# Optimization experiments

Hardware: AMD Instinct MI355X
Metric: run time of the kernel (lower is better)

The kernel has to match this reference:

```python
import jax, jax.numpy as jnp
import numpy as np

B, N, L, D, KQ, OUT = 256, 256, 1024, 256, 64, 64


def setup_inputs() -> dict:
    key = jax.random.key(0)
    ks = jax.random.split(key, 6)
    return {
        "queries": jax.random.normal(ks[0], (B, D), dtype=jnp.float32),
        "keys": jax.random.normal(ks[1], (N, L, D), dtype=jnp.float32),
        "values": jax.random.normal(ks[2], (N, L, D), dtype=jnp.float32),
        "Wq": jax.random.normal(ks[3], (D, KQ), dtype=jnp.float32) * (1.0 / np.sqrt(D)),
        "Wk": jax.random.normal(ks[4], (D, KQ), dtype=jnp.float32) * (1.0 / np.sqrt(D)),
        "Wv": jax.random.normal(ks[5], (D, OUT), dtype=jnp.float32) * (1.0 / np.sqrt(D)),
    }


def reference(queries, keys, values, Wq, Wk, Wv):
    # Projections (bias-free Linear layers)
    q = queries @ Wq                          # [B, KQ]
    k = jnp.einsum('nld,dk->nlk', keys, Wk)   # [N, L, KQ]
    v = jnp.einsum('nld,do->nlo', values, Wv) # [N, L, OUT]
    scale = jnp.asarray(1.0 / np.sqrt(k.shape[-1]), dtype=q.dtype)
    # attn[n, b, l] = q[b] . k[n, l]
    attn = jnp.einsum('bk,nlk->nbl', q, k) * scale
    attn = jax.nn.softmax(attn, axis=-1)      # softmax over protein length L
    # Vectorized version of the per-drug bmm loop: result[b, n, :] = attn[n, b, :] @ v[n]
    result = jnp.einsum('nbl,nlo->bno', attn, v)  # [B, N, OUT]
    return (result, attn)
```

## Files before the change

### kernel.cpp

```cpp
#include <hip/hip_runtime.h>
#include <stdint.h>
#include <stddef.h>

#define B_ 256
#define N_ 256
#define L_ 1024
#define D_ 256
#define KQ_ 64
#define OUT_ 64
#define RESULT_ELEMS (256 * 256 * 64)

typedef __attribute__((ext_vector_type(4))) float f32x4;
typedef __attribute__((ext_vector_type(8))) short s16x8;
typedef __attribute__((ext_vector_type(4))) short s16x4;

__device__ __forceinline__ short f2bf(float f) {
  union { float f; unsigned int u; } v;
  v.f = f;
  unsigned int u = v.u;
  unsigned int r = (u + 0x7FFFu + ((u >> 16) & 1u)) >> 16;
  return (short)r;
}

__global__ void qproj_kernel(const float* __restrict__ queries,
                             const float* __restrict__ Wq,
                             float* __restrict__ qtmp) {
  int b = blockIdx.x * 4 + (threadIdx.x >> 6);
  int j = threadIdx.x & 63;
  float s = 0.f;
#pragma unroll 4
  for (int d = 0; d < D_; ++d)
    s += queries[b * D_ + d] * Wq[d * KQ_ + j];
  qtmp[b * KQ_ + j] = s * 0.125f;
}

__global__ void packq_kernel(const float* __restrict__ qtmp,
                             short* __restrict__ qfrag) {
  int bt = blockIdx.x >> 1, ks = blockIdx.x & 1;
  int lane = threadIdx.x, quad = lane >> 4, l15 = lane & 15;
  s16x8 v;
#pragma unroll
  for (int jj = 0; jj < 8; ++jj)
    v[jj] = f2bf(qtmp[(bt * 16 + l15) * KQ_ + ks * 32 + quad * 8 + jj]);
  *(s16x8*)(qfrag + ((size_t)(bt * 2 + ks) * 64 + lane) * 8) = v;
}

__global__ void packw_kernel(const float* __restrict__ Wk,
                             const float* __restrict__ Wv,
                             short* __restrict__ wkf, short* __restrict__ wvf) {
  int task = blockIdx.x >> 5;
  int ks = (blockIdx.x >> 2) & 7, ct = blockIdx.x & 3;
  const float* W = task ? Wv : Wk;
  short* dst = task ? wvf : wkf;
  int lane = threadIdx.x, quad = lane >> 4, l15 = lane & 15;
  s16x8 v;
#pragma unroll
  for (int jj = 0; jj < 8; ++jj)
    v[jj] = f2bf(W[(ks * 32 + quad * 8 + jj) * 64 + ct * 16 + l15]);
  *(s16x8*)(dst + ((size_t)(ks * 4 + ct) * 64 + lane) * 8) = v;
}

__global__ __launch_bounds__(256) void kvproj_kernel(
    const float* __restrict__ keys, const float* __restrict__ values,
    const short* __restrict__ wkf, const short* __restrict__ wvf,
    short* __restrict__ kfrag, short* __restrict__ vfrag) {
  __shared__ short lbuf[64 * 72];
  int task = blockIdx.y;
  const float* X = task ? values : keys;
  const short* wf = task ? wvf : wkf;
  int m0 = blockIdx.x * 64;
  int w = threadIdx.x >> 6, lane = threadIdx.x & 63;
  int quad = lane >> 4, l15 = lane & 15;

  f32x4 zero = {0.f, 0.f, 0.f, 0.f};
  f32x4 acc[4] = {zero, zero, zero, zero};

  const float* aptr = X + (size_t)(m0 + w * 16 + l15) * D_ + quad * 8;
#pragma unroll
  for (int ks = 0; ks < 8; ++ks) {
    f32x4 a0 = *(const f32x4*)(aptr + ks * 32);
    f32x4 a1 = *(const f32x4*)(aptr + ks * 32 + 4);
    s16x8 af;
#pragma unroll
    for (int jj = 0; jj < 4; ++jj) {
      af[jj] = f2bf(a0[jj]);
      af[jj + 4] = f2bf(a1[jj]);
    }
#pragma unroll
    for (int ct = 0; ct < 4; ++ct) {
      s16x8 bf = *(const s16x8*)(wf + ((size_t)(ks * 4 + ct) * 64 + lane) * 8);
      acc[ct] = __builtin_amdgcn_mfma_f32_16x16x32_bf16(af, bf, acc[ct], 0, 0, 0);
    }
  }

  int n = m0 >> 10, l0 = m0 & 1023;
  if (task == 0) {
#pragma unroll
    for (int ct = 0; ct < 4; ++ct)
#pragma unroll
      for (int r = 0; r < 4; ++r)
        lbuf[(w * 16 + quad * 4 + r) * 72 + ct * 16 + l15] = f2bf(acc[ct][r]);
    __syncthreads();
#pragma unroll
    for (int i = 0; i < 2; ++i) {
      int lt = w, ks = i;
      s16x8 v = *(const s16x8*)&lbuf[(lt * 16 + l15) * 72 + ks * 32 + quad * 8];
      size_t off = (((size_t)(n * 64 + (l0 >> 4) + lt) * 2 + ks) * 64 + lane) * 8;
      *(s16x8*)(kfrag + off) = v;
    }
  } else {
#pragma unroll
    for (int ct = 0; ct < 4; ++ct) {
      s16x4 p;
#pragma unroll
      for (int r = 0; r < 4; ++r) p[r] = f2bf(acc[ct][r]);
      *(s16x4*)&lbuf[(ct * 16 + l15) * 72 + w * 16 + quad * 4] = p;
    }
    __syncthreads();
#pragma unroll
    for (int i = 0; i < 2; ++i) {
      int fid = w * 2 + i, ls = fid >> 2, ot = fid & 3;
      s16x8 v = *(const s16x8*)&lbuf[(ot * 16 + l15) * 72 + ls * 32 + quad * 8];
      size_t off = (((size_t)(n * 32 + (l0 >> 5) + ls) * 4 + ot) * 64 + lane) * 8;
      *(s16x8*)(vfrag + off) = v;
    }
  }
}

__global__ __launch_bounds__(512) void attn_kernel(
    const short* __restrict__ qfrag, const short* __restrict__ kfrag,
    const short* __restrict__ vfrag, float* __restrict__ out) {
  __shared__ short tbuf[8 * 1280];
  int n = blockIdx.x;
  int w = threadIdx.x >> 6, lane = threadIdx.x & 63;
  int quad = lane >> 4, l15 = lane & 15;
  short* tb = tbuf + w * 1280;

  f32x4 zero = {0.f, 0.f, 0.f, 0.f};

  s16x8 qf[2][2];
#pragma unroll
  for (int bt = 0; bt < 2; ++bt)
#pragma unroll
    for (int ks = 0; ks < 2; ++ks)
      qf[bt][ks] = *(const s16x8*)(qfrag +
          ((size_t)((w * 2 + bt) * 2 + ks) * 64 + lane) * 8);

  const short* kb = kfrag + (size_t)n * 65536;
  const short* vb = vfrag + (size_t)n * 65536;

  float se[2][4] = {{0.f, 0.f, 0.f, 0.f}, {0.f, 0.f, 0.f, 0.f}};
#pragma unroll 2
  for (int c = 0; c < 32; ++c) {
    f32x4 S[2][2] = {{zero, zero}, {zero, zero}};
#pragma unroll
    for (int lt = 0; lt < 2; ++lt)
#pragma unroll
      for (int ks = 0; ks < 2; ++ks) {
        s16x8 kf = *(const s16x8*)(kb +
            ((size_t)((c * 2 + lt) * 2 + ks) * 64 + lane) * 8);
#pragma unroll
        for (int bt = 0; bt < 2; ++bt)
          S[bt][lt] = __builtin_amdgcn_mfma_f32_16x16x32_bf16(
              qf[bt][ks], kf, S[bt][lt], 0, 0, 0);
      }
#pragma unroll
    for (int bt = 0; bt < 2; ++bt)
#pragma unroll
      for (int lt = 0; lt < 2; ++lt)
#pragma unroll
        for (int r = 0; r < 4; ++r)
          se[bt][r] += __expf(S[bt][lt][r]);
  }
#pragma unroll
  for (int bt = 0; bt < 2; ++bt)
#pragma unroll
    for (int r = 0; r < 4; ++r) {
      float v = se[bt][r];
      v += __shfl_xor(v, 1);
      v += __shfl_xor(v, 2);
      v += __shfl_xor(v, 4);
      v += __shfl_xor(v, 8);
      se[bt][r] = 1.0f / v;
    }

  f32x4 oacc[2][4] = {{zero, zero, zero, zero}, {zero, zero, zero, zero}};
  float* attnout = out + RESULT_ELEMS + (size_t)n * (B_ * L_);
#pragma unroll 2
  for (int c = 0; c < 32; ++c) {
    f32x4 S[2][2] = {{zero, zero}, {zero, zero}};
#pragma unroll
    for (int lt = 0; lt < 2; ++lt)
#pragma unroll
      for (int ks = 0; ks < 2; ++ks) {
        s16x8 kf = *(const s16x8*)(kb +
            ((size_t)((c * 2 + lt) * 2 + ks) * 64 + lane) * 8);
#pragma unroll
        for (int bt = 0; bt < 2; ++bt)
          S[bt][lt] = __builtin_amdgcn_mfma_f32_16x16x32_bf16(
              qf[bt][ks], kf, S[bt][lt], 0, 0, 0);
      }
#pragma unroll
    for (int bt = 0; bt < 2; ++bt)
#pragma unroll
      for (int lt = 0; lt < 2; ++lt)
#pragma unroll
        for (int r = 0; r < 4; ++r) {
          float p = __expf(S[bt][lt][r]) * se[bt][r];
          int b = w * 32 + bt * 16 + quad * 4 + r;
          int l = c * 32 + lt * 16 + l15;
          attnout[(size_t)b * L_ + l] = p;
          tb[(bt * 16 + quad * 4 + r) * 40 + lt * 16 + l15] = f2bf(p);
        }
    __syncthreads();
    s16x8 af[2];
#pragma unroll
    for (int bt = 0; bt < 2; ++bt)
      af[bt] = *(const s16x8*)&tb[(bt * 16 + l15) * 40 + quad * 8];
#pragma unroll
    for (int ot = 0; ot < 4; ++ot) {
      s16x8 vf = *(const s16x8*)(vb + ((size_t)(c * 4 + ot) * 64 + lane) * 8);
#pragma unroll
      for (int bt = 0; bt < 2; ++bt)
        oacc[bt][ot] = __builtin_amdgcn_mfma_f32_16x16x32_bf16(
            af[bt], vf, oacc[bt][ot], 0, 0, 0);
    }
  }

#pragma unroll
  for (int bt = 0; bt < 2; ++bt)
#pragma unroll
    for (int ot = 0; ot < 4; ++ot)
#pragma unroll
      for (int r = 0; r < 4; ++r) {
        int b = w * 32 + bt * 16 + quad * 4 + r;
        int o = ot * 16 + l15;
        out[((size_t)b * N_ + n) * OUT_ + o] = oacc[bt][ot][r];
      }
}

extern "C" void kernel_launch(void* const* d_in, const int* in_sizes, int n_in,
                              void* d_out, int out_size, void* d_ws, size_t ws_size,
                              hipStream_t stream) {
  const float* queries = (const float*)d_in[0];
  const float* keys    = (const float*)d_in[1];
  const float* values  = (const float*)d_in[2];
  const float* Wq      = (const float*)d_in[3];
  const float* Wk      = (const float*)d_in[4];
  const float* Wv      = (const float*)d_in[5];
  float* out = (float*)d_out;

  char* ws = (char*)d_ws;
  float* qtmp  = (float*)(ws);
  short* qfrag = (short*)(ws + 65536);
  short* wkf   = (short*)(ws + 98304);
  short* wvf   = (short*)(ws + 131072);
  short* kfrag = (short*)(ws + 163840);
  short* vfrag = (short*)(ws + 163840 + 33554432);

  hipLaunchKernelGGL(qproj_kernel, dim3(64), dim3(256), 0, stream, queries, Wq, qtmp);
  hipLaunchKernelGGL(packq_kernel, dim3(32), dim3(64), 0, stream, qtmp, qfrag);
  hipLaunchKernelGGL(packw_kernel, dim3(64), dim3(64), 0, stream, Wk, Wv, wkf, wvf);
  hipLaunchKernelGGL(kvproj_kernel, dim3(4096, 2), dim3(256), 0, stream,
                     keys, values, wkf, wvf, kfrag, vfrag);
  hipLaunchKernelGGL(attn_kernel, dim3(256), dim3(512), 0, stream,
                     qfrag, kfrag, vfrag, out);
}
```

Before: 788.7 us.

## Split attention per drug into four blocks with XCD-aware mapping and exp2 softmax

The attention kernel now launches 1024 blocks of 256 threads instead of 256 blocks of 512. Each wave handles one 16-row query tile instead of two, and block IDs are remapped so the four blocks sharing a drug's K/V land on the same XCD for L2 reuse. The 1/sqrt(KQ) scale now also folds in log2(e), so the kernel can call exp2f instead of __expf. The __syncthreads is replaced by a per-wave lgkmcnt wait with a double-buffered LDS tile, since each wave only reads its own slice. Each K/V tile is now loaded by four blocks rather than one, which depends on L2 hits to avoid extra traffic, but the work is spread over more CUs with higher occupancy.

```diff
diff --git a/kernel.cpp b/kernel.cpp
--- a/kernel.cpp
+++ b/kernel.cpp
@@ -31,7 +31,7 @@
 #pragma unroll 4
   for (int d = 0; d < D_; ++d)
     s += queries[b * D_ + d] * Wq[d * KQ_ + j];
-  qtmp[b * KQ_ + j] = s * 0.125f;
+  qtmp[b * KQ_ + j] = s * 0.18033688011112042f;
 }
 
 __global__ void packq_kernel(const float* __restrict__ qtmp,
@@ -127,116 +127,99 @@
   }
 }
 
-__global__ __launch_bounds__(512) void attn_kernel(
+__global__ __launch_bounds__(256, 4) void attn_kernel(
     const short* __restrict__ qfrag, const short* __restrict__ kfrag,
     const short* __restrict__ vfrag, float* __restrict__ out) {
-  __shared__ short tbuf[8 * 1280];
-  int n = blockIdx.x;
+  __shared__ short tbuf[4 * 2 * 640];
+  int bid = blockIdx.x;
+  int xcd = bid & 7, slot = bid >> 3;
+  int n = xcd * 32 + (slot >> 2);
+  int quarter = slot & 3;
   int w = threadIdx.x >> 6, lane = threadIdx.x & 63;
+  int wg = quarter * 4 + w;
   int quad = lane >> 4, l15 = lane & 15;
-  short* tb = tbuf + w * 1280;
+  short* tb0 = tbuf + w * 1280;
 
   f32x4 zero = {0.f, 0.f, 0.f, 0.f};
 
-  s16x8 qf[2][2];
-#pragma unroll
-  for (int bt = 0; bt < 2; ++bt)
-#pragma unroll
-    for (int ks = 0; ks < 2; ++ks)
-      qf[bt][ks] = *(const s16x8*)(qfrag +
-          ((size_t)((w * 2 + bt) * 2 + ks) * 64 + lane) * 8);
+  s16x8 qf[2];
+#pragma unroll
+  for (int ks = 0; ks < 2; ++ks)
+    qf[ks] = *(const s16x8*)(qfrag + ((size_t)(wg * 2 + ks) * 64 + lane) * 8);
 
   const short* kb = kfrag + (size_t)n * 65536;
   const short* vb = vfrag + (size_t)n * 65536;
 
-  float se[2][4] = {{0.f, 0.f, 0.f, 0.f}, {0.f, 0.f, 0.f, 0.f}};
+  float se[4] = {0.f, 0.f, 0.f, 0.f};
 #pragma unroll 2
   for (int c = 0; c < 32; ++c) {
-    f32x4 S[2][2] = {{zero, zero}, {zero, zero}};
+    f32x4 S[2] = {zero, zero};
 #pragma unroll
     for (int lt = 0; lt < 2; ++lt)
 #pragma unroll
       for (int ks = 0; ks < 2; ++ks) {
         s16x8 kf = *(const s16x8*)(kb +
             ((size_t)((c * 2 + lt) * 2 + ks) * 64 + lane) * 8);
-#pragma unroll
-        for (int bt = 0; bt < 2; ++bt)
-          S[bt][lt] = __builtin_amdgcn_mfma_f32_16x16x32_bf16(
-              qf[bt][ks], kf, S[bt][lt], 0, 0, 0);
+        S[lt] = __builtin_amdgcn_mfma_f32_16x16x32_bf16(qf[ks], kf, S[lt], 0, 0, 0);
       }
 #pragma unroll
-    for (int bt = 0; bt < 2; ++bt)
-#pragma unroll
-      for (int lt = 0; lt < 2; ++lt)
-#pragma unroll
-        for (int r = 0; r < 4; ++r)
-          se[bt][r] += __expf(S[bt][lt][r]);
-  }
-#pragma unroll
-  for (int bt = 0; bt < 2; ++bt)
-#pragma unroll
-    for (int r = 0; r < 4; ++r) {
-      float v = se[bt][r];
-      v += __shfl_xor(v, 1);
-      v += __shfl_xor(v, 2);
-      v += __shfl_xor(v, 4);
-      v += __shfl_xor(v, 8);
-      se[bt][r] = 1.0f / v;
-    }
-
-  f32x4 oacc[2][4] = {{zero, zero, zero, zero}, {zero, zero, zero, zero}};
+    for (int lt = 0; lt < 2; ++lt)
+#pragma unroll
+      for (int r = 0; r < 4; ++r)
+        se[r] += exp2f(S[lt][r]);
+  }
+#pragma unroll
+  for (int r = 0; r < 4; ++r) {
+    float v = se[r];
+    v += __shfl_xor(v, 1);
+    v += __shfl_xor(v, 2);
+    v += __shfl_xor(v, 4);
+    v += __shfl_xor(v, 8);
+    se[r] = 1.0f / v;
+  }
+
+  f32x4 oacc[4] = {zero, zero, zero, zero};
   float* attnout = out + RESULT_ELEMS + (size_t)n * (B_ * L_);
 #pragma unroll 2
   for (int c = 0; c < 32; ++c) {
-    f32x4 S[2][2] = {{zero, zero}, {zero, zero}};
+    short* tb = tb0 + (c & 1) * 640;
+    f32x4 S[2] = {zero, zero};
 #pragma unroll
     for (int lt = 0; lt < 2; ++lt)
 #pragma unroll
       for (int ks = 0; ks < 2; ++ks) {
         s16x8 kf = *(const s16x8*)(kb +
             ((size_t)((c * 2 + lt) * 2 + ks) * 64 + lane) * 8);
-#pragma unroll
-        for (int bt = 0; bt < 2; ++bt)
-          S[bt][lt] = __builtin_amdgcn_mfma_f32_16x16x32_bf16(
-              qf[bt][ks], kf, S[bt][lt], 0, 0, 0);
+        S[lt] = __builtin_amdgcn_mfma_f32_16x16x32_bf16(qf[ks], kf, S[lt], 0, 0, 0);
       }
 #pragma unroll
-    for (int bt = 0; bt < 2; ++bt)
-#pragma unroll
-      for (int lt = 0; lt < 2; ++lt)
-#pragma unroll
-        for (int r = 0; r < 4; ++r) {
-          float p = __expf(S[bt][lt][r]) * se[bt][r];
-          int b = w * 32 + bt * 16 + quad * 4 + r;
-          int l = c * 32 + lt * 16 + l15;
-          attnout[(size_t)b * L_ + l] = p;
-          tb[(bt * 16 + quad * 4 + r) * 40 + lt * 16 + l15] = f2bf(p);
-        }
-    __syncthreads();
-    s16x8 af[2];
-#pragma unroll
-    for (int bt = 0; bt < 2; ++bt)
-      af[bt] = *(const s16x8*)&tb[(bt * 16 + l15) * 40 + quad * 8];
+    for (int lt = 0; lt < 2; ++lt)
+#pragma unroll
+      for (int r = 0; r < 4; ++r) {
+        float p = exp2f(S[lt][r]) * se[r];
+        int b = wg * 16 + quad * 4 + r;
+        int l = c * 32 + lt * 16 + l15;
+        attnout[(size_t)b * L_ + l] = p;
+        tb[(quad * 4 + r) * 40 + lt * 16 + l15] = f2bf(p);
+      }
+    asm volatile("s_waitcnt lgkmcnt(0)" ::: "memory");
+    __builtin_amdgcn_sched_barrier(0);
+    s16x8 af = *(const s16x8*)&tb[l15 * 40 + quad * 8];
 #pragma unroll
     for (int ot = 0; ot < 4; ++ot) {
       s16x8 vf = *(const s16x8*)(vb + ((size_t)(c * 4 + ot) * 64 + lane) * 8);
-#pragma unroll
-      for (int bt = 0; bt < 2; ++bt)
-        oacc[bt][ot] = __builtin_amdgcn_mfma_f32_16x16x32_bf16(
-            af[bt], vf, oacc[bt][ot], 0, 0, 0);
-    }
-  }
-
-#pragma unroll
-  for (int bt = 0; bt < 2; ++bt)
-#pragma unroll
-    for (int ot = 0; ot < 4; ++ot)
-#pragma unroll
-      for (int r = 0; r < 4; ++r) {
-        int b = w * 32 + bt * 16 + quad * 4 + r;
-        int o = ot * 16 + l15;
-        out[((size_t)b * N_ + n) * OUT_ + o] = oacc[bt][ot][r];
-      }
+      oacc[ot] = __builtin_amdgcn_mfma_f32_16x16x32_bf16(af, vf, oacc[ot], 0, 0, 0);
+    }
+  }
+
+#pragma unroll
+  for (int ot = 0; ot < 4; ++ot)
+#pragma unroll
+    for (int r = 0; r < 4; ++r) {
+      int b = wg * 16 + quad * 4 + r;
+      int o = ot * 16 + l15;
+      out[((size_t)b * N_ + n) * OUT_ + o] = oacc[ot][r];
+    }
 }
 
 extern "C" void kernel_launch(void* const* d_in, const int* in_sizes, int n_in,
@@ -263,6 +246,6 @@
   hipLaunchKernelGGL(packw_kernel, dim3(64), dim3(64), 0, stream, Wk, Wv, wkf, wvf);
   hipLaunchKernelGGL(kvproj_kernel, dim3(4096, 2), dim3(256), 0, stream,
                      keys, values, wkf, wvf, kfrag, vfrag);
-  hipLaunchKernelGGL(attn_kernel, dim3(256), dim3(512), 0, stream,
+  hipLaunchKernelGGL(attn_kernel, dim3(1024), dim3(256), 0, stream,
                      qfrag, kfrag, vfrag, out);
 }
```

Result: no change. 773.9 us (-1.9%).
